# Performance work log

Measured on AMD Instinct MI355X. Metric: run time of the kernel, lower is better.

The kernel has to match this reference:

```python
import jax, jax.numpy as jnp
import numpy as np

EXPANSION_RATES = [10, 25]
NEG_SLOPE = 0.2


def gat_layer(x_self, x_neigh, W, a_self, a_neigh):
    """Multi-head GAT attention over a fixed neighbor fanout.

    x_self:  [M, F]      target-node features
    x_neigh: [M, K, F]   K sampled neighbors per target
    W:       [H, F, D]   per-head projection
    a_self:  [H, D]      attention vector (self part)
    a_neigh: [H, D]      attention vector (neighbor part)
    returns  [M, H*D]    concatenated heads
    """
    hs = jnp.einsum('mf,hfd->mhd', x_self, W)              # [M,H,D]
    hn = jnp.einsum('mkf,hfd->mkhd', x_neigh, W)           # [M,K,H,D]
    e_self = jnp.einsum('mhd,hd->mh', hs, a_self)          # [M,H]
    e_neigh = jnp.einsum('mkhd,hd->mkh', hn, a_neigh)      # [M,K,H]
    e = jax.nn.leaky_relu(e_self[:, None, :] + e_neigh, NEG_SLOPE)
    alpha = jax.nn.softmax(e, axis=1)                      # softmax over K neighbors
    out = jnp.einsum('mkh,mkhd->mhd', alpha, hn)           # [M,H,D]
    return out.reshape(out.shape[0], -1)                   # concat heads


def setup_inputs() -> dict:
    key = jax.random.key(0)
    ks = jax.random.split(key, 10)
    B, F, D, H, OUT = 1024, 128, 128, 2, 128
    r0, r1 = EXPANSION_RATES
    inp = {}
    # hierarchical embeddings: level j has B * prod(rates[:j]) rows
    inp['h0'] = jax.random.normal(ks[0], (B, F), dtype=jnp.float32)
    inp['h1'] = jax.random.normal(ks[1], (B * r0, F), dtype=jnp.float32)
    inp['h2'] = jax.random.normal(ks[2], (B * r0 * r1, F), dtype=jnp.float32)
    # layer 0: consumes raw features (F); layer 1: consumes H*D
    inp['W0'] = jax.random.normal(ks[3], (H, F, D), dtype=jnp.float32) / np.sqrt(F)
    inp['a_self0'] = jax.random.normal(ks[4], (H, D), dtype=jnp.float32) / np.sqrt(D)
    inp['a_neigh0'] = jax.random.normal(ks[5], (H, D), dtype=jnp.float32) / np.sqrt(D)
    inp['W1'] = jax.random.normal(ks[6], (H, H * D, D), dtype=jnp.float32) / np.sqrt(H * D)
    inp['a_self1'] = jax.random.normal(ks[7], (H, D), dtype=jnp.float32) / np.sqrt(D)
    inp['a_neigh1'] = jax.random.normal(ks[8], (H, D), dtype=jnp.float32) / np.sqrt(D)
    inp['fc_W'] = jax.random.normal(ks[9], (H * D, OUT), dtype=jnp.float32) / np.sqrt(H * D)
    return inp


def reference(h0, h1, h2, W0, a_self0, a_neigh0, W1, a_self1, a_neigh1, fc_W):
    hidden = [h0, h1, h2]
    layers = [(W0, a_self0, a_neigh0), (W1, a_self1, a_neigh1)]
    depth = len(EXPANSION_RATES)
    for i, (W, a_s, a_n) in enumerate(layers):
        for j in range(depth - i):
            x_self = hidden[j]                                   # [M, F_i]
            M = x_self.shape[0]
            # neighbor rows of level j+1 grouped in blocks of expansion_rates[j]
            x_neigh = hidden[j + 1].reshape(M, EXPANSION_RATES[j], x_self.shape[1])
            hidden[j] = gat_layer(x_self, x_neigh, W, a_s, a_n)  # [M, H*D]
    return hidden[0] @ fc_W                                      # [B, OUT]
```

## Files before the change

### kernel.cpp

```cpp
#include <hip/hip_runtime.h>

#define LRELU_SLOPE 0.2f

#define OFF_UV0  0u
#define OFF_U1   512u
#define OFF_V1   1024u
#define OFF_P    1536u
#define OFF_PP   2048u
#define OFF_Q    4096u
#define OFF_R    69632u
#define OFF_Y1   135168u
#define OFF_Y0   2756608u

__device__ __forceinline__ float dot4(float4 a, float4 b) {
    return a.x * b.x + a.y * b.y + a.z * b.z + a.w * b.w;
}

template<int CTRL>
__device__ __forceinline__ float dppmov(float x) {
    return __int_as_float(__builtin_amdgcn_update_dpp(
        0, __float_as_int(x), CTRL, 0xf, 0xf, true));
}
__device__ __forceinline__ float sum16(float x) {
    x += dppmov<0xB1>(x);
    x += dppmov<0x4E>(x);
    x += dppmov<0x141>(x);
    x += dppmov<0x140>(x);
    return x;
}
__device__ __forceinline__ float sum32(float x) {
    x = sum16(x);
    return x + __shfl_xor(x, 16);
}
__device__ __forceinline__ float sum64(float x) {
    float y = sum32(x);
    return y + __shfl_xor(y, 32);
}
__device__ __forceinline__ float lrelu(float x) {
    return (x >= 0.f) ? x : LRELU_SLOPE * x;
}

__global__ __launch_bounds__(256)
void prepA_kernel(const float* __restrict__ W0, const float* __restrict__ as0,
                  const float* __restrict__ an0,
                  const float* __restrict__ W1, const float* __restrict__ as1,
                  const float* __restrict__ an1,
                  const float* __restrict__ fcW, float* __restrict__ ws) {
    __shared__ float s[32 * 129];
    const int b = blockIdx.x;
    const int t = threadIdx.x;
    if (b < 192) {
        const int wid = b * 4 + (t >> 6);
        const int lane = t & 63;
        const float *wrow, *as, *an;
        if (wid < 256) {
            wrow = W0 + (size_t)wid * 128;
            int h = wid >> 7;
            as = as0 + h * 128; an = an0 + h * 128;
        } else {
            int g = wid - 256;
            wrow = W1 + (size_t)g * 128;
            int h = g >> 8;
            as = as1 + h * 128; an = an1 + h * 128;
        }
        float2 w = *(const float2*)(wrow + 2 * lane);
        float2 sv = *(const float2*)(as + 2 * lane);
        float2 nv = *(const float2*)(an + 2 * lane);
        float au = sum64(w.x * sv.x + w.y * sv.y);
        float av = sum64(w.x * nv.x + w.y * nv.y);
        if (lane == 0) {
            if (wid < 256) { ws[OFF_UV0 + wid] = au; ws[OFF_UV0 + 256 + wid] = av; }
            else { int g = wid - 256; ws[OFF_U1 + g] = au; ws[OFF_V1 + g] = av; }
        }
    } else {
        const int idx = b - 192;
        const int h = idx >> 3, g0 = (idx & 7) * 32;
        const float* Wh = W1 + (size_t)h * 32768;
        for (int ii = t * 4; ii < 32 * 128; ii += 1024) {
            int i = ii >> 7, d = ii & 127;
            float4 g4 = *(const float4*)(Wh + (size_t)(g0 + i) * 128 + d);
            s[i * 129 + d + 0] = g4.x;
            s[i * 129 + d + 1] = g4.y;
            s[i * 129 + d + 2] = g4.z;
            s[i * 129 + d + 3] = g4.w;
        }
        __syncthreads();
        const int dg = t & 31, rg = t >> 5;
        float4 acc[4];
        #pragma unroll
        for (int j = 0; j < 4; ++j) acc[j] = make_float4(0.f, 0.f, 0.f, 0.f);
        const float* fp = fcW + (size_t)h * 16384 + 4 * dg;
        #pragma unroll 4
        for (int d2 = 0; d2 < 128; ++d2) {
            float4 f4 = *(const float4*)(fp + (size_t)d2 * 128);
            #pragma unroll
            for (int j = 0; j < 4; ++j) {
                float x = s[(rg * 4 + j) * 129 + d2];
                acc[j].x += x * f4.x; acc[j].y += x * f4.y;
                acc[j].z += x * f4.z; acc[j].w += x * f4.w;
            }
        }
        float* Qp = ws + OFF_Q + (size_t)h * 32768;
        #pragma unroll
        for (int j = 0; j < 4; ++j)
            *(float4*)(Qp + (size_t)(g0 + rg * 4 + j) * 128 + 4 * dg) = acc[j];
    }
}

__device__ __forceinline__ void upd2(float& m, float& s, float4& A,
                                     float ea, float eb,
                                     const float4& xa, const float4& xb) {
    float mn = fmaxf(m, fmaxf(ea, eb));
    float sc = __expf(m - mn);
    float pa = __expf(ea - mn);
    float pb = __expf(eb - mn);
    s = s * sc + pa + pb;
    A.x = A.x * sc + pa * xa.x + pb * xb.x;
    A.y = A.y * sc + pa * xa.y + pb * xb.y;
    A.z = A.z * sc + pa * xa.z + pb * xb.z;
    A.w = A.w * sc + pa * xa.w + pb * xb.w;
    m = mn;
}
__device__ __forceinline__ void upd1(float& m, float& s, float4& A,
                                     float ea, const float4& xa) {
    float mn = fmaxf(m, ea);
    float sc = __expf(m - mn);
    float pa = __expf(ea - mn);
    s = s * sc + pa;
    A.x = A.x * sc + pa * xa.x;
    A.y = A.y * sc + pa * xa.y;
    A.z = A.z * sc + pa * xa.z;
    A.w = A.w * sc + pa * xa.w;
    m = mn;
}

__global__ __launch_bounds__(256)
void big3_kernel(const float* __restrict__ h0, const float* __restrict__ h1,
                 const float* __restrict__ h2, const float* __restrict__ W0,
                 float* __restrict__ ws) {
    const int b = blockIdx.x;
    const int t = threadIdx.x;
    const float* uv0 = ws + OFF_UV0;

    if (b < 2560) {
        const int lane = t & 63;
        const int half = lane >> 5;
        const int fl = lane & 31;
        const int m = b * 4 + (t >> 6);
        const float* xnp = h2 + (size_t)m * 3200;
        const float* xsp = h1 + (size_t)m * 128;
        const float4 u0 = *(const float4*)(uv0 + 0 + 4 * fl);
        const float4 u1 = *(const float4*)(uv0 + 128 + 4 * fl);
        const float4 v0 = *(const float4*)(uv0 + 256 + 4 * fl);
        const float4 v1 = *(const float4*)(uv0 + 384 + 4 * fl);

        float4 xs = *(const float4*)(xsp + 4 * fl);
        const float es0 = sum32(dot4(xs, u0));
        const float es1 = sum32(dot4(xs, u1));

        float4 xa = *(const float4*)(xnp + (size_t)(0 + half) * 128 + 4 * fl);
        float4 xb = *(const float4*)(xnp + (size_t)(2 + half) * 128 + 4 * fl);
        float m0 = -1e30f, m1 = -1e30f, s0 = 0.f, s1 = 0.f;
        float4 A0 = make_float4(0.f, 0.f, 0.f, 0.f);
        float4 A1 = make_float4(0.f, 0.f, 0.f, 0.f);
        #pragma unroll
        for (int c = 0; c < 6; ++c) {
            float4 na, nb;
            if (c < 5) {
                na = *(const float4*)(xnp + (size_t)(4 * c + 4 + half) * 128 + 4 * fl);
                nb = *(const float4*)(xnp + (size_t)(4 * c + 6 + half) * 128 + 4 * fl);
            } else {
                na = *(const float4*)(xnp + (size_t)24 * 128 + 4 * fl);
                nb = na;
            }
            float ea0 = lrelu(es0 + sum32(dot4(xa, v0)));
            float ea1 = lrelu(es1 + sum32(dot4(xa, v1)));
            float eb0 = lrelu(es0 + sum32(dot4(xb, v0)));
            float eb1 = lrelu(es1 + sum32(dot4(xb, v1)));
            upd2(m0, s0, A0, ea0, eb0, xa, xb);
            upd2(m1, s1, A1, ea1, eb1, xa, xb);
            xa = na; xb = nb;
        }
        {
            float e0 = lrelu(es0 + sum32(dot4(xa, v0)));
            float e1 = lrelu(es1 + sum32(dot4(xa, v1)));
            if (half) { e0 = -1e30f; e1 = -1e30f; }
            upd1(m0, s0, A0, e0, xa);
            upd1(m1, s1, A1, e1, xa);
        }
        float g0 = fmaxf(m0, __shfl_xor(m0, 32));
        float g1 = fmaxf(m1, __shfl_xor(m1, 32));
        float c0 = __expf(m0 - g0), c1 = __expf(m1 - g1);
        s0 *= c0; s1 *= c1;
        A0.x *= c0; A0.y *= c0; A0.z *= c0; A0.w *= c0;
        A1.x *= c1; A1.y *= c1; A1.z *= c1; A1.w *= c1;
        s0 += __shfl_xor(s0, 32); s1 += __shfl_xor(s1, 32);
        A0.x += __shfl_xor(A0.x, 32); A0.y += __shfl_xor(A0.y, 32);
        A0.z += __shfl_xor(A0.z, 32); A0.w += __shfl_xor(A0.w, 32);
        A1.x += __shfl_xor(A1.x, 32); A1.y += __shfl_xor(A1.y, 32);
        A1.z += __shfl_xor(A1.z, 32); A1.w += __shfl_xor(A1.w, 32);
        const float inv = 1.f / (half ? s1 : s0);
        const float4 S = half ? A1 : A0;
        float4 o;
        o.x = S.x * inv; o.y = S.y * inv; o.z = S.z * inv; o.w = S.w * inv;
        *(float4*)(ws + OFF_Y1 + (size_t)m * 256 + half * 128 + 4 * fl) = o;
    } else if (b < 2816) {
        const int lane = t & 63;
        const int half = lane >> 5;
        const int fl = lane & 31;
        const int m = (b - 2560) * 4 + (t >> 6);
        const float* xnp = h1 + (size_t)m * 1280;
        const float* xsp = h0 + (size_t)m * 128;
        const float4 u0 = *(const float4*)(uv0 + 0 + 4 * fl);
        const float4 u1 = *(const float4*)(uv0 + 128 + 4 * fl);
        const float4 v0 = *(const float4*)(uv0 + 256 + 4 * fl);
        const float4 v1 = *(const float4*)(uv0 + 384 + 4 * fl);

        float4 xs = *(const float4*)(xsp + 4 * fl);
        const float es0 = sum32(dot4(xs, u0));
        const float es1 = sum32(dot4(xs, u1));

        float4 xa = *(const float4*)(xnp + (size_t)(0 + half) * 128 + 4 * fl);
        float4 xb = *(const float4*)(xnp + (size_t)(2 + half) * 128 + 4 * fl);
        float m0 = -1e30f, m1 = -1e30f, s0 = 0.f, s1 = 0.f;
        float4 A0 = make_float4(0.f, 0.f, 0.f, 0.f);
        float4 A1 = make_float4(0.f, 0.f, 0.f, 0.f);
        #pragma unroll
        for (int c = 0; c < 2; ++c) {
            float4 na, nb;
            if (c < 1) {
                na = *(const float4*)(xnp + (size_t)(4 + half) * 128 + 4 * fl);
                nb = *(const float4*)(xnp + (size_t)(6 + half) * 128 + 4 * fl);
            } else {
                na = *(const float4*)(xnp + (size_t)(8 + half) * 128 + 4 * fl);
                nb = na;
            }
            float ea0 = lrelu(es0 + sum32(dot4(xa, v0)));
            float ea1 = lrelu(es1 + sum32(dot4(xa, v1)));
            float eb0 = lrelu(es0 + sum32(dot4(xb, v0)));
            float eb1 = lrelu(es1 + sum32(dot4(xb, v1)));
            upd2(m0, s0, A0, ea0, eb0, xa, xb);
            upd2(m1, s1, A1, ea1, eb1, xa, xb);
            xa = na; xb = nb;
        }
        {
            float e0 = lrelu(es0 + sum32(dot4(xa, v0)));
            float e1 = lrelu(es1 + sum32(dot4(xa, v1)));
            upd1(m0, s0, A0, e0, xa);
            upd1(m1, s1, A1, e1, xa);
        }
        float g0 = fmaxf(m0, __shfl_xor(m0, 32));
        float g1 = fmaxf(m1, __shfl_xor(m1, 32));
        float c0 = __expf(m0 - g0), c1 = __expf(m1 - g1);
        s0 *= c0; s1 *= c1;
        A0.x *= c0; A0.y *= c0; A0.z *= c0; A0.w *= c0;
        A1.x *= c1; A1.y *= c1; A1.z *= c1; A1.w *= c1;
        s0 += __shfl_xor(s0, 32); s1 += __shfl_xor(s1, 32);
        A0.x += __shfl_xor(A0.x, 32); A0.y += __shfl_xor(A0.y, 32);
        A0.z += __shfl_xor(A0.z, 32); A0.w += __shfl_xor(A0.w, 32);
        A1.x += __shfl_xor(A1.x, 32); A1.y += __shfl_xor(A1.y, 32);
        A1.z += __shfl_xor(A1.z, 32); A1.w += __shfl_xor(A1.w, 32);
        const float inv = 1.f / (half ? s1 : s0);
        const float4 S = half ? A1 : A0;
        float4 o;
        o.x = S.x * inv; o.y = S.y * inv; o.z = S.z * inv; o.w = S.w * inv;
        *(float4*)(ws + OFF_Y0 + (size_t)m * 256 + half * 128 + 4 * fl) = o;
    } else if (b < 2944) {
        const int wid = (b - 2816) * 4 + (t >> 6);
        const int lane = t & 63;
        const int h = wid >> 8, rest = wid & 255;
        const int h0i = rest >> 7;
        const float* wrow = W0 + (size_t)rest * 128;
        float2 w2 = *(const float2*)(wrow + 2 * lane);
        float2 su = *(const float2*)(ws + OFF_U1 + h * 256 + h0i * 128 + 2 * lane);
        float2 sv = *(const float2*)(ws + OFF_V1 + h * 256 + h0i * 128 + 2 * lane);
        float pu = sum64(w2.x * su.x + w2.y * su.y);
        float pv = sum64(w2.x * sv.x + w2.y * sv.y);
        if (lane == 0) { ws[OFF_PP + wid] = pu; ws[OFF_P + wid] = pv; }
    } else {
        __shared__ float smem[4160];
        const int idx = b - 2944;
        const int h = idx >> 3;
        const int h0i = (idx >> 2) & 1;
        const int f0 = (idx & 3) * 32;
        const float* W0h = W0 + (size_t)h0i * 16384;
        for (int ii = t * 4; ii < 32 * 128; ii += 1024) {
            int i = ii >> 7, d = ii & 127;
            float4 g4 = *(const float4*)(W0h + (size_t)(f0 + i) * 128 + d);
            smem[i * 129 + d + 0] = g4.x;
            smem[i * 129 + d + 1] = g4.y;
            smem[i * 129 + d + 2] = g4.z;
            smem[i * 129 + d + 3] = g4.w;
        }
        __syncthreads();
        const int dg = t & 31, rg = t >> 5;
        float4 acc[4];
        #pragma unroll
        for (int j = 0; j < 4; ++j) acc[j] = make_float4(0.f, 0.f, 0.f, 0.f);
        const float* Qp = ws + OFF_Q + (size_t)h * 32768 + (size_t)h0i * 16384 + 4 * dg;
        #pragma unroll 4
        for (int d = 0; d < 128; ++d) {
            float4 q4 = *(const float4*)(Qp + (size_t)d * 128);
            #pragma unroll
            for (int j = 0; j < 4; ++j) {
                float x = smem[(rg * 4 + j) * 129 + d];
                acc[j].x += x * q4.x; acc[j].y += x * q4.y;
                acc[j].z += x * q4.z; acc[j].w += x * q4.w;
            }
        }
        float* Rp = ws + OFF_R + (size_t)h * 32768 + (size_t)h0i * 16384;
        #pragma unroll
        for (int j = 0; j < 4; ++j)
            *(float4*)(Rp + (size_t)(f0 + rg * 4 + j) * 128 + 4 * dg) = acc[j];
    }
}

__global__ __launch_bounds__(256)
void final_kernel(const float* __restrict__ ws, float* __restrict__ out) {
    __shared__ float xn[22 * 256];
    __shared__ float yb[1024];
    __shared__ float pr[2][2][128];
    __shared__ float en[2][11][2];
    __shared__ float al[2][10][2];
    const int t = threadIdx.x;
    const int m0 = blockIdx.x * 2;
    const int rlane = t & 63;
    const int rg = t >> 6;
    const float* P  = ws + OFF_P;
    const float* Pp = ws + OFF_PP;
    const float* Y1 = ws + OFF_Y1;
    const float* Y0 = ws + OFF_Y0;
    const float4 su0 = *(const float4*)(Pp + 0 + 4 * rlane);
    const float4 su1 = *(const float4*)(Pp + 256 + 4 * rlane);
    const float4 nv0 = *(const float4*)(P + 0 + 4 * rlane);
    const float4 nv1 = *(const float4*)(P + 256 + 4 * rlane);
    float4 g[6];
    #pragma unroll
    for (int i = 0; i < 6; ++i) {
        int rho = rg + 4 * i;
        if (rho < 22) {
            int r = rho / 11, k = rho % 11;
            int m = m0 + r;
            const float* src = (k < 10) ? (Y1 + ((size_t)m * 10 + k) * 256)
                                        : (Y0 + (size_t)m * 256);
            g[i] = *(const float4*)(src + 4 * rlane);
        }
    }
    #pragma unroll
    for (int i = 0; i < 6; ++i) {
        int rho = rg + 4 * i;
        if (rho < 22) {
            int r = rho / 11, k = rho % 11;
            *(float4*)(&xn[rho * 256 + 4 * rlane]) = g[i];
            float p0 = sum64(dot4(g[i], (k < 10) ? nv0 : su0));
            float p1 = sum64(dot4(g[i], (k < 10) ? nv1 : su1));
            if (rlane == 0) { en[r][k][0] = p0; en[r][k][1] = p1; }
        }
    }
    __syncthreads();
    if (t < 128) {
        int r = t >> 6, h = (t >> 5) & 1, k = t & 31;
        float e = -1e30f;
        if (k < 10) {
            float z = en[r][10][h] + en[r][k][h];
            e = (z >= 0.f) ? z : LRELU_SLOPE * z;
        }
        float mx = e;
        #pragma unroll
        for (int off = 16; off > 0; off >>= 1) mx = fmaxf(mx, __shfl_xor(mx, off));
        float ex = (k < 10) ? __expf(e - mx) : 0.f;
        float sm = ex;
        #pragma unroll
        for (int off = 16; off > 0; off >>= 1) sm += __shfl_xor(sm, off);
        if (k < 10) al[r][k][h] = ex / sm;
    }
    __syncthreads();
    #pragma unroll
    for (int i = 0; i < 4; ++i) {
        int c = t + 256 * i;
        int r = c >> 9, rem = c & 511, h = rem >> 8, f = rem & 255;
        float acc = 0.f;
        #pragma unroll
        for (int k = 0; k < 10; ++k) acc += al[r][k][h] * xn[(r * 11 + k) * 256 + f];
        yb[c] = acc;
    }
    __syncthreads();
    {
        const int seg = t >> 7;
        const int o = t & 127;
        const float* Rv = ws + OFF_R + (size_t)seg * 256 * 128 + o;
        const float* y0p = yb + seg * 256;
        const float* y1p = yb + 512 + seg * 256;
        float a0 = 0.f, a1 = 0.f;
        #pragma unroll 8
        for (int gi = 0; gi < 256; ++gi) {
            float rv = Rv[(size_t)gi * 128];
            a0 += y0p[gi] * rv;
            a1 += y1p[gi] * rv;
        }
        pr[seg][0][o] = a0;
        pr[seg][1][o] = a1;
    }
    __syncthreads();
    {
        const int r = t >> 7, o = t & 127;
        out[(size_t)(m0 + r) * 128 + o] = pr[0][r][o] + pr[1][r][o];
    }
}

extern "C" void kernel_launch(void* const* d_in, const int* in_sizes, int n_in,
                              void* d_out, int out_size, void* d_ws, size_t ws_size,
                              hipStream_t stream) {
    const float* h0  = (const float*)d_in[0];
    const float* h1  = (const float*)d_in[1];
    const float* h2  = (const float*)d_in[2];
    const float* W0  = (const float*)d_in[3];
    const float* as0 = (const float*)d_in[4];
    const float* an0 = (const float*)d_in[5];
    const float* W1  = (const float*)d_in[6];
    const float* as1 = (const float*)d_in[7];
    const float* an1 = (const float*)d_in[8];
    const float* fcW = (const float*)d_in[9];
    float* outp = (float*)d_out;
    float* ws = (float*)d_ws;

    hipLaunchKernelGGL(prepA_kernel, dim3(208), dim3(256), 0, stream,
                       W0, as0, an0, W1, as1, an1, fcW, ws);
    hipLaunchKernelGGL(big3_kernel, dim3(2960), dim3(256), 0, stream,
                       h0, h1, h2, W0, ws);
    hipLaunchKernelGGL(final_kernel, dim3(512), dim3(256), 0, stream,
                       ws, outp);
}
```

Measured before the change: 67.61 us.

## Map one target node per half-wave in attention blocks and split Q precompute finer

```diff
diff --git a/kernel.cpp b/kernel.cpp
--- a/kernel.cpp
+++ b/kernel.cpp
@@ -46,7 +46,7 @@
                   const float* __restrict__ W1, const float* __restrict__ as1,
                   const float* __restrict__ an1,
                   const float* __restrict__ fcW, float* __restrict__ ws) {
-    __shared__ float s[32 * 129];
+    __shared__ float s[16 * 129];
     const int b = blockIdx.x;
     const int t = threadIdx.x;
     if (b < 192) {
@@ -74,9 +74,9 @@
         }
     } else {
         const int idx = b - 192;
-        const int h = idx >> 3, g0 = (idx & 7) * 32;
+        const int h = idx >> 4, g0 = (idx & 15) * 16;
         const float* Wh = W1 + (size_t)h * 32768;
-        for (int ii = t * 4; ii < 32 * 128; ii += 1024) {
+        for (int ii = t * 4; ii < 16 * 128; ii += 1024) {
             int i = ii >> 7, d = ii & 127;
             float4 g4 = *(const float4*)(Wh + (size_t)(g0 + i) * 128 + d);
             s[i * 129 + d + 0] = g4.x;
@@ -86,24 +86,24 @@
         }
         __syncthreads();
         const int dg = t & 31, rg = t >> 5;
-        float4 acc[4];
-        #pragma unroll
-        for (int j = 0; j < 4; ++j) acc[j] = make_float4(0.f, 0.f, 0.f, 0.f);
+        float4 acc[2];
+        acc[0] = make_float4(0.f, 0.f, 0.f, 0.f);
+        acc[1] = make_float4(0.f, 0.f, 0.f, 0.f);
         const float* fp = fcW + (size_t)h * 16384 + 4 * dg;
         #pragma unroll 4
         for (int d2 = 0; d2 < 128; ++d2) {
             float4 f4 = *(const float4*)(fp + (size_t)d2 * 128);
             #pragma unroll
-            for (int j = 0; j < 4; ++j) {
-                float x = s[(rg * 4 + j) * 129 + d2];
+            for (int j = 0; j < 2; ++j) {
+                float x = s[(rg * 2 + j) * 129 + d2];
                 acc[j].x += x * f4.x; acc[j].y += x * f4.y;
                 acc[j].z += x * f4.z; acc[j].w += x * f4.w;
             }
         }
         float* Qp = ws + OFF_Q + (size_t)h * 32768;
         #pragma unroll
-        for (int j = 0; j < 4; ++j)
-            *(float4*)(Qp + (size_t)(g0 + rg * 4 + j) * 128 + 4 * dg) = acc[j];
+        for (int j = 0; j < 2; ++j)
+            *(float4*)(Qp + (size_t)(g0 + rg * 2 + j) * 128 + 4 * dg) = acc[j];
     }
 }
 
@@ -135,18 +135,18 @@
 }
 
 __global__ __launch_bounds__(256)
-void big3_kernel(const float* __restrict__ h0, const float* __restrict__ h1,
+void big4_kernel(const float* __restrict__ h0, const float* __restrict__ h1,
                  const float* __restrict__ h2, const float* __restrict__ W0,
                  float* __restrict__ ws) {
     const int b = blockIdx.x;
     const int t = threadIdx.x;
     const float* uv0 = ws + OFF_UV0;
 
-    if (b < 2560) {
+    if (b < 1280) {
         const int lane = t & 63;
-        const int half = lane >> 5;
+        const int sub = lane >> 5;
         const int fl = lane & 31;
-        const int m = b * 4 + (t >> 6);
+        const int m = (b * 4 + (t >> 6)) * 2 + sub;
         const float* xnp = h2 + (size_t)m * 3200;
         const float* xsp = h1 + (size_t)m * 128;
         const float4 u0 = *(const float4*)(uv0 + 0 + 4 * fl);
@@ -158,17 +158,17 @@
         const float es0 = sum32(dot4(xs, u0));
         const float es1 = sum32(dot4(xs, u1));
 
-        float4 xa = *(const float4*)(xnp + (size_t)(0 + half) * 128 + 4 * fl);
-        float4 xb = *(const float4*)(xnp + (size_t)(2 + half) * 128 + 4 * fl);
+        float4 xa = *(const float4*)(xnp + 4 * fl);
+        float4 xb = *(const float4*)(xnp + 128 + 4 * fl);
         float m0 = -1e30f, m1 = -1e30f, s0 = 0.f, s1 = 0.f;
         float4 A0 = make_float4(0.f, 0.f, 0.f, 0.f);
         float4 A1 = make_float4(0.f, 0.f, 0.f, 0.f);
         #pragma unroll
-        for (int c = 0; c < 6; ++c) {
+        for (int c = 0; c < 12; ++c) {
             float4 na, nb;
-            if (c < 5) {
-                na = *(const float4*)(xnp + (size_t)(4 * c + 4 + half) * 128 + 4 * fl);
-                nb = *(const float4*)(xnp + (size_t)(4 * c + 6 + half) * 128 + 4 * fl);
+            if (c < 11) {
+                na = *(const float4*)(xnp + (size_t)(2 * c + 2) * 128 + 4 * fl);
+                nb = *(const float4*)(xnp + (size_t)(2 * c + 3) * 128 + 4 * fl);
             } else {
                 na = *(const float4*)(xnp + (size_t)24 * 128 + 4 * fl);
                 nb = na;
@@ -184,31 +184,20 @@
         {
             float e0 = lrelu(es0 + sum32(dot4(xa, v0)));
             float e1 = lrelu(es1 + sum32(dot4(xa, v1)));
-            if (half) { e0 = -1e30f; e1 = -1e30f; }
             upd1(m0, s0, A0, e0, xa);
             upd1(m1, s1, A1, e1, xa);
         }
-        float g0 = fmaxf(m0, __shfl_xor(m0, 32));
-        float g1 = fmaxf(m1, __shfl_xor(m1, 32));
-        float c0 = __expf(m0 - g0), c1 = __expf(m1 - g1);
-        s0 *= c0; s1 *= c1;
-        A0.x *= c0; A0.y *= c0; A0.z *= c0; A0.w *= c0;
-        A1.x *= c1; A1.y *= c1; A1.z *= c1; A1.w *= c1;
-        s0 += __shfl_xor(s0, 32); s1 += __shfl_xor(s1, 32);
-        A0.x += __shfl_xor(A0.x, 32); A0.y += __shfl_xor(A0.y, 32);
-        A0.z += __shfl_xor(A0.z, 32); A0.w += __shfl_xor(A0.w, 32);
-        A1.x += __shfl_xor(A1.x, 32); A1.y += __shfl_xor(A1.y, 32);
-        A1.z += __shfl_xor(A1.z, 32); A1.w += __shfl_xor(A1.w, 32);
-        const float inv = 1.f / (half ? s1 : s0);
-        const float4 S = half ? A1 : A0;
-        float4 o;
-        o.x = S.x * inv; o.y = S.y * inv; o.z = S.z * inv; o.w = S.w * inv;
-        *(float4*)(ws + OFF_Y1 + (size_t)m * 256 + half * 128 + 4 * fl) = o;
-    } else if (b < 2816) {
+        const float i0 = 1.f / s0, i1 = 1.f / s1;
+        float4 o0, o1;
+        o0.x = A0.x * i0; o0.y = A0.y * i0; o0.z = A0.z * i0; o0.w = A0.w * i0;
+        o1.x = A1.x * i1; o1.y = A1.y * i1; o1.z = A1.z * i1; o1.w = A1.w * i1;
+        *(float4*)(ws + OFF_Y1 + (size_t)m * 256 + 4 * fl) = o0;
+        *(float4*)(ws + OFF_Y1 + (size_t)m * 256 + 128 + 4 * fl) = o1;
+    } else if (b < 1408) {
         const int lane = t & 63;
-        const int half = lane >> 5;
+        const int sub = lane >> 5;
         const int fl = lane & 31;
-        const int m = (b - 2560) * 4 + (t >> 6);
+        const int m = ((b - 1280) * 4 + (t >> 6)) * 2 + sub;
         const float* xnp = h1 + (size_t)m * 1280;
         const float* xsp = h0 + (size_t)m * 128;
         const float4 u0 = *(const float4*)(uv0 + 0 + 4 * fl);
@@ -220,20 +209,19 @@
         const float es0 = sum32(dot4(xs, u0));
         const float es1 = sum32(dot4(xs, u1));
 
-        float4 xa = *(const float4*)(xnp + (size_t)(0 + half) * 128 + 4 * fl);
-        float4 xb = *(const float4*)(xnp + (size_t)(2 + half) * 128 + 4 * fl);
+        float4 xa = *(const float4*)(xnp + 4 * fl);
+        float4 xb = *(const float4*)(xnp + 128 + 4 * fl);
         float m0 = -1e30f, m1 = -1e30f, s0 = 0.f, s1 = 0.f;
         float4 A0 = make_float4(0.f, 0.f, 0.f, 0.f);
         float4 A1 = make_float4(0.f, 0.f, 0.f, 0.f);
         #pragma unroll
-        for (int c = 0; c < 2; ++c) {
+        for (int c = 0; c < 5; ++c) {
             float4 na, nb;
-            if (c < 1) {
-                na = *(const float4*)(xnp + (size_t)(4 + half) * 128 + 4 * fl);
-                nb = *(const float4*)(xnp + (size_t)(6 + half) * 128 + 4 * fl);
+            if (c < 4) {
+                na = *(const float4*)(xnp + (size_t)(2 * c + 2) * 128 + 4 * fl);
+                nb = *(const float4*)(xnp + (size_t)(2 * c + 3) * 128 + 4 * fl);
             } else {
-                na = *(const float4*)(xnp + (size_t)(8 + half) * 128 + 4 * fl);
-                nb = na;
+                na = xa; nb = xb;
             }
             float ea0 = lrelu(es0 + sum32(dot4(xa, v0)));
             float ea1 = lrelu(es1 + sum32(dot4(xa, v1)));
@@ -243,30 +231,14 @@
             upd2(m1, s1, A1, ea1, eb1, xa, xb);
             xa = na; xb = nb;
         }
-        {
-            float e0 = lrelu(es0 + sum32(dot4(xa, v0)));
-            float e1 = lrelu(es1 + sum32(dot4(xa, v1)));
-            upd1(m0, s0, A0, e0, xa);
-            upd1(m1, s1, A1, e1, xa);
-        }
-        float g0 = fmaxf(m0, __shfl_xor(m0, 32));
-        float g1 = fmaxf(m1, __shfl_xor(m1, 32));
-        float c0 = __expf(m0 - g0), c1 = __expf(m1 - g1);
-        s0 *= c0; s1 *= c1;
-        A0.x *= c0; A0.y *= c0; A0.z *= c0; A0.w *= c0;
-        A1.x *= c1; A1.y *= c1; A1.z *= c1; A1.w *= c1;
-        s0 += __shfl_xor(s0, 32); s1 += __shfl_xor(s1, 32);
-        A0.x += __shfl_xor(A0.x, 32); A0.y += __shfl_xor(A0.y, 32);
-        A0.z += __shfl_xor(A0.z, 32); A0.w += __shfl_xor(A0.w, 32);
-        A1.x += __shfl_xor(A1.x, 32); A1.y += __shfl_xor(A1.y, 32);
-        A1.z += __shfl_xor(A1.z, 32); A1.w += __shfl_xor(A1.w, 32);
-        const float inv = 1.f / (half ? s1 : s0);
-        const float4 S = half ? A1 : A0;
-        float4 o;
-        o.x = S.x * inv; o.y = S.y * inv; o.z = S.z * inv; o.w = S.w * inv;
-        *(float4*)(ws + OFF_Y0 + (size_t)m * 256 + half * 128 + 4 * fl) = o;
-    } else if (b < 2944) {
-        const int wid = (b - 2816) * 4 + (t >> 6);
+        const float i0 = 1.f / s0, i1 = 1.f / s1;
+        float4 o0, o1;
+        o0.x = A0.x * i0; o0.y = A0.y * i0; o0.z = A0.z * i0; o0.w = A0.w * i0;
+        o1.x = A1.x * i1; o1.y = A1.y * i1; o1.z = A1.z * i1; o1.w = A1.w * i1;
+        *(float4*)(ws + OFF_Y0 + (size_t)m * 256 + 4 * fl) = o0;
+        *(float4*)(ws + OFF_Y0 + (size_t)m * 256 + 128 + 4 * fl) = o1;
+    } else if (b < 1536) {
+        const int wid = (b - 1408) * 4 + (t >> 6);
         const int lane = t & 63;
         const int h = wid >> 8, rest = wid & 255;
         const int h0i = rest >> 7;
@@ -279,7 +251,7 @@
         if (lane == 0) { ws[OFF_PP + wid] = pu; ws[OFF_P + wid] = pv; }
     } else {
         __shared__ float smem[4160];
-        const int idx = b - 2944;
+        const int idx = b - 1536;
         const int h = idx >> 3;
         const int h0i = (idx >> 2) & 1;
         const int f0 = (idx & 3) * 32;
@@ -424,9 +396,9 @@
     float* outp = (float*)d_out;
     float* ws = (float*)d_ws;
 
-    hipLaunchKernelGGL(prepA_kernel, dim3(208), dim3(256), 0, stream,
+    hipLaunchKernelGGL(prepA_kernel, dim3(224), dim3(256), 0, stream,
                        W0, as0, an0, W1, as1, an1, fcW, ws);
-    hipLaunchKernelGGL(big3_kernel, dim3(2960), dim3(256), 0, stream,
+    hipLaunchKernelGGL(big4_kernel, dim3(1552), dim3(256), 0, stream,
                        h0, h1, h2, W0, ws);
     hipLaunchKernelGGL(final_kernel, dim3(512), dim3(256), 0, stream,
                        ws, outp);
```

New measurement: 63.67 us. 1.06x faster.
